# Performance work log

Measured on AMD Instinct MI355X. Metric: run time of the kernel, lower is better.

Reference implementation:

```python
import jax, jax.numpy as jnp
import numpy as np

# Neuron hyperparameters (mid-range of the optuna search space)
THRESHOLD = 1.0
CURRENT_DECAY = 0.3
VOLTAGE_DECAY = 0.8
TAU_GRAD = 0.5
SCALE_GRAD = 1.0

B, N_IN, H, N_OUT, T = 64, 2048, 1024, 2, 128
SPIKE_RATE = 0.1  # input spike density


@jax.custom_vjp
def spike_fn(v):
    # Heaviside spike with SLAYER exponential surrogate gradient
    return (v >= 0.0).astype(v.dtype)

def _spike_fwd(v):
    return spike_fn(v), v

def _spike_bwd(v, g):
    return (g * SCALE_GRAD * jnp.exp(-jnp.abs(v) / TAU_GRAD),)

spike_fn.defvjp(_spike_fwd, _spike_bwd)


def cuba_dense(spike, W):
    """One SLAYER CUBA Dense block: dense synapse + leaky IF neuron over time.
    spike: [B, N_in, T], W: [N_out, N_in] -> [B, N_out, T] output spikes."""
    z = jnp.einsum('oi,bit->tbo', W, spike)  # synaptic current input, [T, B, O]
    O = W.shape[0]
    zeros = jnp.zeros((spike.shape[0], O), spike.dtype)

    def step(carry, z_t):
        cur, vol = carry
        cur = cur * (1.0 - CURRENT_DECAY) + z_t          # current dynamics
        vol = vol * (1.0 - VOLTAGE_DECAY) + cur          # voltage dynamics
        s = spike_fn(vol - THRESHOLD)                    # threshold spike
        vol = vol * (1.0 - s)                            # reset to zero on spike
        return (cur, vol), s

    _, s = jax.lax.scan(step, (zeros, zeros), z)
    return jnp.transpose(s, (1, 2, 0))  # [B, O, T]


def setup_inputs() -> dict:
    key = jax.random.key(0)
    k0, k1, k2, k3 = jax.random.split(key, 4)
    spike = (jax.random.uniform(k0, (B, N_IN, T)) < SPIKE_RATE).astype(jnp.float32)
    W1 = jax.random.normal(k1, (H, N_IN), jnp.float32) / np.sqrt(N_IN).astype(np.float32)
    W2 = jax.random.normal(k2, (H, H), jnp.float32) / np.sqrt(H).astype(np.float32)
    W3 = jax.random.normal(k3, (N_OUT, H), jnp.float32) / np.sqrt(H).astype(np.float32)
    return {"spike": spike, "W1": W1, "W2": W2, "W3": W3}


def reference(spike, W1, W2, W3):
    s = cuba_dense(spike, W1)
    s = cuba_dense(s, W2)
    s = cuba_dense(s, W3)
    return s  # [B, 2, T]
```

## Files before the change

### kernel.cpp

```cpp
#include <hip/hip_runtime.h>


typedef unsigned short ushort_t;
typedef unsigned int uint_t;
typedef __bf16 bf16x8 __attribute__((ext_vector_type(8)));
typedef float f32x4 __attribute__((ext_vector_type(4)));

#define O_TOT 1024

__device__ __forceinline__ void glds16(const ushort_t* g, ushort_t* l) {
  __builtin_amdgcn_global_load_lds(
      (const __attribute__((address_space(1))) uint_t*)g,
      (__attribute__((address_space(3))) uint_t*)l, 16, 0, 0);
}

__device__ __forceinline__ ushort_t f32_to_bf16_rne(float f) {
  uint_t u = __float_as_uint(f);
  u += 0x7FFFu + ((u >> 16) & 1u);
  return (ushort_t)(u >> 16);
}

__global__ __launch_bounds__(256) void prep(const float* __restrict__ W1,
                                            const float* __restrict__ W2,
                                            const float* __restrict__ spike,
                                            ushort_t* __restrict__ h1,
                                            ushort_t* __restrict__ l1,
                                            ushort_t* __restrict__ h2,
                                            ushort_t* __restrict__ l2,
                                            ushort_t* __restrict__ A1) {
  const int tid = threadIdx.x;
  if (blockIdx.x < 12288) {
    const float* W;
    ushort_t *hp, *lp;
    int idx, K;
    if (blockIdx.x < 8192) {
      idx = blockIdx.x * 256 + tid;
      W = W1; hp = h1; lp = l1; K = 2048;
    } else {
      idx = (blockIdx.x - 8192) * 256 + tid;
      W = W2; hp = h2; lp = l2; K = 1024;
    }
    int e = idx & 7, fr = (idx >> 3) & 15, q = (idx >> 7) & 3;
    int kk = (idx >> 9) & 1, j = (idx >> 10) & 1, qn = (idx >> 11) & 1;
    int rest = idx >> 12;
    int kcm = (K == 2048) ? 31 : 15;
    int kcs = (K == 2048) ? 5 : 4;
    int kc = rest & kcm, o_blk = rest >> kcs;
    int o = o_blk * 64 + qn * 32 + j * 16 + fr;
    int k = kc * 64 + kk * 32 + q * 8 + e;
    float w = W[(size_t)o * K + k];
    ushort_t h = f32_to_bf16_rne(w);
    hp[idx] = h;
    lp[idx] = f32_to_bf16_rne(w - __uint_as_float(((uint_t)h) << 16));
    return;
  }
  __shared__ ushort_t lds[128 * 130];
  const int bid = blockIdx.x - 12288;
  const int b = bid >> 4;
  const int i0 = (bid & 15) * 128;
#pragma unroll
  for (int it = 0; it < 16; ++it) {
    int p = it * 256 + tid;
    int i = p >> 5, tg = (p & 31) * 4;
    float4 v = *(const float4*)(spike + ((size_t)b * 2048 + i0 + i) * 128 + tg);
    lds[i * 130 + tg + 0] = (v.x != 0.0f) ? 0x3F80u : 0u;
    lds[i * 130 + tg + 1] = (v.y != 0.0f) ? 0x3F80u : 0u;
    lds[i * 130 + tg + 2] = (v.z != 0.0f) ? 0x3F80u : 0u;
    lds[i * 130 + tg + 3] = (v.w != 0.0f) ? 0x3F80u : 0u;
  }
  __syncthreads();
#pragma unroll
  for (int it = 0; it < 16; ++it) {
    int p = it * 256 + tid;
    int t = p >> 5, j = p & 31;
    uint_t u0 = (uint_t)lds[(4 * j + 0) * 130 + t] | ((uint_t)lds[(4 * j + 1) * 130 + t] << 16);
    uint_t u1 = (uint_t)lds[(4 * j + 2) * 130 + t] | ((uint_t)lds[(4 * j + 3) * 130 + t] << 16);
    uint2* dst = (uint2*)(A1 + (size_t)(b * 128 + t) * 2048 + i0);
    dst[j] = make_uint2(u0, u1);
  }
}

__global__ __launch_bounds__(256, 4)
void gemm_scan(const ushort_t* __restrict__ A, const ushort_t* __restrict__ Bhp,
               const ushort_t* __restrict__ Blp, ushort_t* __restrict__ S,
               int K) {
  __shared__ float smemf[128 * 65];
  ushort_t* As = (ushort_t*)smemf;
  float* Zt = smemf;

  const int tid = threadIdx.x;
  const int wave = tid >> 6, lane = tid & 63;
  const int b = blockIdx.y;
  const int m0 = b * 128;
  const int o0 = blockIdx.x * 64;
  const int qm = wave >> 1, qn = wave & 1;
  const int fr = lane & 15, q = lane >> 4;

  f32x4 acc[4][2];
#pragma unroll
  for (int i = 0; i < 4; ++i)
#pragma unroll
    for (int j = 0; j < 2; ++j) acc[i][j] = (f32x4){0.f, 0.f, 0.f, 0.f};

  size_t gA[4];
  ushort_t* lA[4];
#pragma unroll
  for (int r = 0; r < 4; ++r) {
    int s = wave * 256 + r * 64 + lane;
    int row = s >> 3;
    int u = (s & 7) ^ (row & 7);
    gA[r] = (size_t)(m0 + row) * K + u * 8;
    lA[r] = As + (size_t)(wave * 256 + r * 64) * 8;
  }

  int aoff[4][2];
#pragma unroll
  for (int i = 0; i < 4; ++i)
#pragma unroll
    for (int kk = 0; kk < 2; ++kk) {
      int row = qm * 64 + i * 16 + fr;
      aoff[i][kk] = row * 64 + (((kk * 4 + q) ^ (row & 7))) * 8;
    }

  const size_t pbase = ((size_t)blockIdx.x * (K >> 6)) * 4096 + qn * 2048 + lane * 8;
  const ushort_t* pBh = Bhp + pbase;
  const ushort_t* pBl = Blp + pbase;

  for (int kc = 0; kc < K; kc += 64) {
    bf16x8 bh[2][2], bl[2][2];
    const ushort_t* ph = pBh + (size_t)(kc >> 6) * 4096;
    const ushort_t* pl = pBl + (size_t)(kc >> 6) * 4096;
#pragma unroll
    for (int j = 0; j < 2; ++j)
#pragma unroll
      for (int kk = 0; kk < 2; ++kk) {
        bh[j][kk] = *(const bf16x8*)(ph + j * 1024 + kk * 512);
        bl[j][kk] = *(const bf16x8*)(pl + j * 1024 + kk * 512);
      }
#pragma unroll
    for (int r = 0; r < 4; ++r) glds16(A + gA[r] + kc, lA[r]);
    __syncthreads();

#pragma unroll
    for (int kk = 0; kk < 2; ++kk) {
      bf16x8 af[4];
#pragma unroll
      for (int i = 0; i < 4; ++i) af[i] = *(const bf16x8*)(As + aoff[i][kk]);
#pragma unroll
      for (int i = 0; i < 4; ++i)
#pragma unroll
        for (int j = 0; j < 2; ++j) {
          acc[i][j] = __builtin_amdgcn_mfma_f32_16x16x32_bf16(af[i], bh[j][kk], acc[i][j], 0, 0, 0);
          acc[i][j] = __builtin_amdgcn_mfma_f32_16x16x32_bf16(af[i], bl[j][kk], acc[i][j], 0, 0, 0);
        }
    }
    __syncthreads();
  }

#pragma unroll
  for (int i = 0; i < 4; ++i)
#pragma unroll
    for (int j = 0; j < 2; ++j)
#pragma unroll
      for (int rr = 0; rr < 4; ++rr)
        Zt[(qm * 64 + i * 16 + q * 4 + rr) * 65 + qn * 32 + j * 16 + fr] = acc[i][j][rr];
  __syncthreads();

  if (tid < 64) {
#pragma clang fp contract(off)
    float cur = 0.0f, vol = 0.0f;
    const int o = o0 + tid;
    for (int t = 0; t < 128; ++t) {
      float z = Zt[t * 65 + tid];
      cur = cur * 0.7f;
      cur = cur + z;
      vol = vol * 0.2f;
      vol = vol + cur;
      float v = vol - 1.0f;
      float s = (v >= 0.0f) ? 1.0f : 0.0f;
      vol = vol * (1.0f - s);
      S[(size_t)(m0 + t) * O_TOT + o] = (v >= 0.0f) ? 0x3F80u : 0u;
    }
  }
}

__global__ __launch_bounds__(256) void gemm3_scan(const ushort_t* __restrict__ X,
                                                  const float* __restrict__ W3,
                                                  float* __restrict__ out) {
  __shared__ float w3s[2048];
  __shared__ float z3[256];
  __shared__ float sp[256];
  const int tid = threadIdx.x;
  const int b = blockIdx.x;
  for (int i = tid; i < 2048; i += 256) w3s[i] = W3[i];
  __syncthreads();
  const int wave = tid >> 6, lane = tid & 63;
  for (int tt = 0; tt < 32; ++tt) {
    int t = wave * 32 + tt;
    const uint_t* row = (const uint_t*)(X + (size_t)(b * 128 + t) * 1024) + lane * 8;
    float s0 = 0.0f, s1 = 0.0f;
#pragma unroll
    for (int jw = 0; jw < 8; ++jw) {
      uint_t u = row[jw];
      float x0 = __uint_as_float(u << 16);
      float x1 = __uint_as_float(u & 0xFFFF0000u);
      int i0 = lane * 16 + jw * 2;
      s0 = fmaf(x0, w3s[i0], s0);
      s1 = fmaf(x0, w3s[1024 + i0], s1);
      s0 = fmaf(x1, w3s[i0 + 1], s0);
      s1 = fmaf(x1, w3s[1024 + i0 + 1], s1);
    }
#pragma unroll
    for (int off = 32; off > 0; off >>= 1) {
      s0 += __shfl_down(s0, off);
      s1 += __shfl_down(s1, off);
    }
    if (lane == 0) {
      z3[t * 2] = s0;
      z3[t * 2 + 1] = s1;
    }
  }
  __syncthreads();
  if (tid < 2) {
#pragma clang fp contract(off)
    float cur = 0.0f, vol = 0.0f;
    for (int t = 0; t < 128; ++t) {
      float z = z3[t * 2 + tid];
      cur = cur * 0.7f;
      cur = cur + z;
      vol = vol * 0.2f;
      vol = vol + cur;
      float v = vol - 1.0f;
      float s = (v >= 0.0f) ? 1.0f : 0.0f;
      vol = vol * (1.0f - s);
      sp[tid * 128 + t] = s;
    }
  }
  __syncthreads();
  out[b * 256 + tid] = sp[tid];
}

extern "C" void kernel_launch(void* const* d_in, const int* in_sizes, int n_in,
                              void* d_out, int out_size, void* d_ws, size_t ws_size,
                              hipStream_t stream) {
  const float* spike = (const float*)d_in[0];
  const float* W1 = (const float*)d_in[1];
  const float* W2 = (const float*)d_in[2];
  const float* W3 = (const float*)d_in[3];
  float* out = (float*)d_out;

  char* ws = (char*)d_ws;
  ushort_t* A1 = (ushort_t*)ws;
  ushort_t* S2 = (ushort_t*)(ws + (size_t)32 * 1024 * 1024);
  ushort_t* S3 = (ushort_t*)(ws + (size_t)48 * 1024 * 1024);
  ushort_t* W1hi = (ushort_t*)(ws + (size_t)64 * 1024 * 1024);
  ushort_t* W1lo = (ushort_t*)(ws + (size_t)68 * 1024 * 1024);
  ushort_t* W2hi = (ushort_t*)(ws + (size_t)72 * 1024 * 1024);
  ushort_t* W2lo = (ushort_t*)(ws + (size_t)74 * 1024 * 1024);

  prep<<<13312, 256, 0, stream>>>(W1, W2, spike, W1hi, W1lo, W2hi, W2lo, A1);
  gemm_scan<<<dim3(16, 64), 256, 0, stream>>>(A1, W1hi, W1lo, S2, 2048);
  gemm_scan<<<dim3(16, 64), 256, 0, stream>>>(S2, W2hi, W2lo, S3, 1024);
  gemm3_scan<<<64, 256, 0, stream>>>(S3, W3, out);
}
```

Measured before the change: 251.5 us.

## Switch spike GEMMs to int8 MFMA with three-plane weight decomposition

Binary spike activations are stored as uint8 instead of bf16, and weights are split into three int8 fixed-point planes (scales 2^-8, 2^-15, 2^-22) instead of bf16 hi/lo pairs. The GEMMs use i32 16x16x64 int8 MFMA and recombine the planes in fp32 before the scan. This halves activation bytes and raises MFMA throughput. The trade-offs are three MFMAs per tile instead of two, output tiles shrinking to 32 columns, and exactness that now depends on weight magnitude fitting the int8 range (|w|<0.5) and on quantization residuals small enough not to flip spike thresholds.

New measurement: 236.7 us. -5.9%, faster.

```diff
diff --git a/kernel.cpp b/kernel.cpp
--- a/kernel.cpp
+++ b/kernel.cpp
@@ -3,59 +3,62 @@
 
 typedef unsigned short ushort_t;
 typedef unsigned int uint_t;
-typedef __bf16 bf16x8 __attribute__((ext_vector_type(8)));
-typedef float f32x4 __attribute__((ext_vector_type(4)));
-
-#define O_TOT 1024
-
-__device__ __forceinline__ void glds16(const ushort_t* g, ushort_t* l) {
+typedef unsigned char uchar_t;
+typedef int i32x4 __attribute__((ext_vector_type(4)));
+
+#define S1F 0.00390625f
+#define S2F 3.0517578125e-5f
+#define S3F 2.384185791015625e-7f
+
+__device__ __forceinline__ void glds16(const uchar_t* g, uchar_t* l) {
   __builtin_amdgcn_global_load_lds(
       (const __attribute__((address_space(1))) uint_t*)g,
       (__attribute__((address_space(3))) uint_t*)l, 16, 0, 0);
 }
 
-__device__ __forceinline__ ushort_t f32_to_bf16_rne(float f) {
-  uint_t u = __float_as_uint(f);
-  u += 0x7FFFu + ((u >> 16) & 1u);
-  return (ushort_t)(u >> 16);
-}
-
 __global__ __launch_bounds__(256) void prep(const float* __restrict__ W1,
                                             const float* __restrict__ W2,
                                             const float* __restrict__ spike,
-                                            ushort_t* __restrict__ h1,
-                                            ushort_t* __restrict__ l1,
-                                            ushort_t* __restrict__ h2,
-                                            ushort_t* __restrict__ l2,
-                                            ushort_t* __restrict__ A1) {
+                                            char* __restrict__ w1q1,
+                                            char* __restrict__ w1q2,
+                                            char* __restrict__ w1q3,
+                                            char* __restrict__ w2q1,
+                                            char* __restrict__ w2q2,
+                                            char* __restrict__ w2q3,
+                                            uchar_t* __restrict__ A1) {
   const int tid = threadIdx.x;
-  if (blockIdx.x < 12288) {
+  if (blockIdx.x < 3072) {
     const float* W;
-    ushort_t *hp, *lp;
-    int idx, K;
-    if (blockIdx.x < 8192) {
-      idx = blockIdx.x * 256 + tid;
-      W = W1; hp = h1; lp = l1; K = 2048;
+    char *p1, *p2, *p3;
+    size_t e0;
+    if (blockIdx.x < 2048) {
+      W = W1; p1 = w1q1; p2 = w1q2; p3 = w1q3;
+      e0 = (size_t)blockIdx.x * 1024 + tid * 4;
     } else {
-      idx = (blockIdx.x - 8192) * 256 + tid;
-      W = W2; hp = h2; lp = l2; K = 1024;
-    }
-    int e = idx & 7, fr = (idx >> 3) & 15, q = (idx >> 7) & 3;
-    int kk = (idx >> 9) & 1, j = (idx >> 10) & 1, qn = (idx >> 11) & 1;
-    int rest = idx >> 12;
-    int kcm = (K == 2048) ? 31 : 15;
-    int kcs = (K == 2048) ? 5 : 4;
-    int kc = rest & kcm, o_blk = rest >> kcs;
-    int o = o_blk * 64 + qn * 32 + j * 16 + fr;
-    int k = kc * 64 + kk * 32 + q * 8 + e;
-    float w = W[(size_t)o * K + k];
-    ushort_t h = f32_to_bf16_rne(w);
-    hp[idx] = h;
-    lp[idx] = f32_to_bf16_rne(w - __uint_as_float(((uint_t)h) << 16));
+      W = W2; p1 = w2q1; p2 = w2q2; p3 = w2q3;
+      e0 = (size_t)(blockIdx.x - 2048) * 1024 + tid * 4;
+    }
+    float4 w = *(const float4*)(W + e0);
+    char4 c1, c2, c3;
+    float q, r;
+#define QUANT(comp, f1, f2, f3)                    \
+    q = rintf((comp) * 256.0f);  f1 = (char)(int)q; \
+    r = (comp) - q * S1F;                           \
+    q = rintf(r * 32768.0f);     f2 = (char)(int)q; \
+    r = r - q * S2F;                                \
+    q = rintf(r * 4194304.0f);   f3 = (char)(int)q;
+    QUANT(w.x, c1.x, c2.x, c3.x)
+    QUANT(w.y, c1.y, c2.y, c3.y)
+    QUANT(w.z, c1.z, c2.z, c3.z)
+    QUANT(w.w, c1.w, c2.w, c3.w)
+#undef QUANT
+    *(char4*)(p1 + e0) = c1;
+    *(char4*)(p2 + e0) = c2;
+    *(char4*)(p3 + e0) = c3;
     return;
   }
-  __shared__ ushort_t lds[128 * 130];
-  const int bid = blockIdx.x - 12288;
+  __shared__ uchar_t lds8[128 * 132];
+  const int bid = blockIdx.x - 3072;
   const int b = bid >> 4;
   const int i0 = (bid & 15) * 128;
 #pragma unroll
@@ -63,115 +66,116 @@
     int p = it * 256 + tid;
     int i = p >> 5, tg = (p & 31) * 4;
     float4 v = *(const float4*)(spike + ((size_t)b * 2048 + i0 + i) * 128 + tg);
-    lds[i * 130 + tg + 0] = (v.x != 0.0f) ? 0x3F80u : 0u;
-    lds[i * 130 + tg + 1] = (v.y != 0.0f) ? 0x3F80u : 0u;
-    lds[i * 130 + tg + 2] = (v.z != 0.0f) ? 0x3F80u : 0u;
-    lds[i * 130 + tg + 3] = (v.w != 0.0f) ? 0x3F80u : 0u;
+    uint_t pk = (v.x != 0.0f ? 1u : 0u) | (v.y != 0.0f ? 1u : 0u) << 8 |
+                (v.z != 0.0f ? 1u : 0u) << 16 | (v.w != 0.0f ? 1u : 0u) << 24;
+    *(uint_t*)(lds8 + i * 132 + tg) = pk;
   }
   __syncthreads();
 #pragma unroll
   for (int it = 0; it < 16; ++it) {
     int p = it * 256 + tid;
-    int t = p >> 5, j = p & 31;
-    uint_t u0 = (uint_t)lds[(4 * j + 0) * 130 + t] | ((uint_t)lds[(4 * j + 1) * 130 + t] << 16);
-    uint_t u1 = (uint_t)lds[(4 * j + 2) * 130 + t] | ((uint_t)lds[(4 * j + 3) * 130 + t] << 16);
-    uint2* dst = (uint2*)(A1 + (size_t)(b * 128 + t) * 2048 + i0);
-    dst[j] = make_uint2(u0, u1);
+    int t = p >> 5, jw = p & 31;
+    uint_t u = (uint_t)lds8[(4 * jw + 0) * 132 + t] |
+               ((uint_t)lds8[(4 * jw + 1) * 132 + t] << 8) |
+               ((uint_t)lds8[(4 * jw + 2) * 132 + t] << 16) |
+               ((uint_t)lds8[(4 * jw + 3) * 132 + t] << 24);
+    *(uint_t*)(A1 + (size_t)(b * 128 + t) * 2048 + i0 + jw * 4) = u;
   }
 }
 
 __global__ __launch_bounds__(256, 4)
-void gemm_scan(const ushort_t* __restrict__ A, const ushort_t* __restrict__ Bhp,
-               const ushort_t* __restrict__ Blp, ushort_t* __restrict__ S,
-               int K) {
-  __shared__ float smemf[128 * 65];
-  ushort_t* As = (ushort_t*)smemf;
+void gemm_scan(const uchar_t* __restrict__ A, const char* __restrict__ Q1,
+               const char* __restrict__ Q2, const char* __restrict__ Q3,
+               uchar_t* __restrict__ S, int K) {
+  __shared__ float smemf[128 * 33];
+  uchar_t* sA = (uchar_t*)smemf;
   float* Zt = smemf;
 
   const int tid = threadIdx.x;
   const int wave = tid >> 6, lane = tid & 63;
-  const int b = blockIdx.y;
-  const int m0 = b * 128;
-  const int o0 = blockIdx.x * 64;
+  const int m0 = blockIdx.y * 128;
+  const int o0 = blockIdx.x * 32;
   const int qm = wave >> 1, qn = wave & 1;
   const int fr = lane & 15, q = lane >> 4;
 
-  f32x4 acc[4][2];
+  i32x4 acc[4][3];
 #pragma unroll
   for (int i = 0; i < 4; ++i)
 #pragma unroll
-    for (int j = 0; j < 2; ++j) acc[i][j] = (f32x4){0.f, 0.f, 0.f, 0.f};
-
-  size_t gA[4];
-  ushort_t* lA[4];
-#pragma unroll
-  for (int r = 0; r < 4; ++r) {
-    int s = wave * 256 + r * 64 + lane;
-    int row = s >> 3;
-    int u = (s & 7) ^ (row & 7);
-    gA[r] = (size_t)(m0 + row) * K + u * 8;
-    lA[r] = As + (size_t)(wave * 256 + r * 64) * 8;
-  }
-
-  int aoff[4][2];
+    for (int p = 0; p < 3; ++p) acc[i][p] = (i32x4){0, 0, 0, 0};
+
+  const char* qplanes[3] = {Q1, Q2, Q3};
+  const uchar_t* gsrc[4];
+  uchar_t* ldst[4];
+#pragma unroll
+  for (int it = 0; it < 4; ++it) {
+    int s = it * 256 + tid;
+    gsrc[it] = nullptr;
+    if (s < 896) {
+      ldst[it] = sA + (size_t)(it * 256 + wave * 64) * 16;
+      if (s < 512) {
+        int row = s >> 2, pu = s & 3;
+        int u = pu ^ ((row >> 1) & 3);
+        gsrc[it] = A + (size_t)(m0 + row) * K + u * 16;
+      } else {
+        int t2 = s - 512;
+        int p = t2 >> 7, r = t2 & 127;
+        int row = r >> 2, pu = r & 3;
+        int u = pu ^ ((row >> 1) & 3);
+        gsrc[it] = (const uchar_t*)qplanes[p] + (size_t)(o0 + row) * K + u * 16;
+      }
+    }
+  }
+
+  int aoff[4], boff[3];
+#pragma unroll
+  for (int i = 0; i < 4; ++i) {
+    int row = qm * 64 + i * 16 + fr;
+    aoff[i] = (row * 4 + (q ^ ((row >> 1) & 3))) * 16;
+  }
+  {
+    int row = qn * 16 + fr;
+    int phys = (row * 4 + (q ^ ((row >> 1) & 3))) * 16;
+#pragma unroll
+    for (int p = 0; p < 3; ++p) boff[p] = 8192 + p * 2048 + phys;
+  }
+
+  for (int kc = 0; kc < K; kc += 64) {
+#pragma unroll
+    for (int it = 0; it < 4; ++it)
+      if (gsrc[it]) glds16(gsrc[it] + kc, ldst[it]);
+    __syncthreads();
+
+    i32x4 af[4], bq[3];
+#pragma unroll
+    for (int i = 0; i < 4; ++i) af[i] = *(const i32x4*)(sA + aoff[i]);
+#pragma unroll
+    for (int p = 0; p < 3; ++p) bq[p] = *(const i32x4*)(sA + boff[p]);
+#pragma unroll
+    for (int p = 0; p < 3; ++p)
+#pragma unroll
+      for (int i = 0; i < 4; ++i)
+        acc[i][p] = __builtin_amdgcn_mfma_i32_16x16x64_i8(af[i], bq[p], acc[i][p], 0, 0, 0);
+    __syncthreads();
+  }
+
 #pragma unroll
   for (int i = 0; i < 4; ++i)
 #pragma unroll
-    for (int kk = 0; kk < 2; ++kk) {
-      int row = qm * 64 + i * 16 + fr;
-      aoff[i][kk] = row * 64 + (((kk * 4 + q) ^ (row & 7))) * 8;
-    }
-
-  const size_t pbase = ((size_t)blockIdx.x * (K >> 6)) * 4096 + qn * 2048 + lane * 8;
-  const ushort_t* pBh = Bhp + pbase;
-  const ushort_t* pBl = Blp + pbase;
-
-  for (int kc = 0; kc < K; kc += 64) {
-    bf16x8 bh[2][2], bl[2][2];
-    const ushort_t* ph = pBh + (size_t)(kc >> 6) * 4096;
-    const ushort_t* pl = pBl + (size_t)(kc >> 6) * 4096;
-#pragma unroll
-    for (int j = 0; j < 2; ++j)
-#pragma unroll
-      for (int kk = 0; kk < 2; ++kk) {
-        bh[j][kk] = *(const bf16x8*)(ph + j * 1024 + kk * 512);
-        bl[j][kk] = *(const bf16x8*)(pl + j * 1024 + kk * 512);
-      }
-#pragma unroll
-    for (int r = 0; r < 4; ++r) glds16(A + gA[r] + kc, lA[r]);
-    __syncthreads();
-
-#pragma unroll
-    for (int kk = 0; kk < 2; ++kk) {
-      bf16x8 af[4];
-#pragma unroll
-      for (int i = 0; i < 4; ++i) af[i] = *(const bf16x8*)(As + aoff[i][kk]);
-#pragma unroll
-      for (int i = 0; i < 4; ++i)
-#pragma unroll
-        for (int j = 0; j < 2; ++j) {
-          acc[i][j] = __builtin_amdgcn_mfma_f32_16x16x32_bf16(af[i], bh[j][kk], acc[i][j], 0, 0, 0);
-          acc[i][j] = __builtin_amdgcn_mfma_f32_16x16x32_bf16(af[i], bl[j][kk], acc[i][j], 0, 0, 0);
-        }
-    }
-    __syncthreads();
-  }
-
-#pragma unroll
-  for (int i = 0; i < 4; ++i)
-#pragma unroll
-    for (int j = 0; j < 2; ++j)
-#pragma unroll
-      for (int rr = 0; rr < 4; ++rr)
-        Zt[(qm * 64 + i * 16 + q * 4 + rr) * 65 + qn * 32 + j * 16 + fr] = acc[i][j][rr];
-  __syncthreads();
-
-  if (tid < 64) {
+    for (int rr = 0; rr < 4; ++rr) {
+      int t = qm * 64 + i * 16 + q * 4 + rr;
+      float z = (float)acc[i][0][rr] * S1F + (float)acc[i][1][rr] * S2F +
+                (float)acc[i][2][rr] * S3F;
+      Zt[t * 33 + qn * 16 + fr] = z;
+    }
+  __syncthreads();
+
+  if (tid < 32) {
 #pragma clang fp contract(off)
     float cur = 0.0f, vol = 0.0f;
     const int o = o0 + tid;
     for (int t = 0; t < 128; ++t) {
-      float z = Zt[t * 65 + tid];
+      float z = Zt[t * 33 + tid];
       cur = cur * 0.7f;
       cur = cur + z;
       vol = vol * 0.2f;
@@ -179,12 +183,12 @@
       float v = vol - 1.0f;
       float s = (v >= 0.0f) ? 1.0f : 0.0f;
       vol = vol * (1.0f - s);
-      S[(size_t)(m0 + t) * O_TOT + o] = (v >= 0.0f) ? 0x3F80u : 0u;
-    }
-  }
-}
-
-__global__ __launch_bounds__(256) void gemm3_scan(const ushort_t* __restrict__ X,
+      S[(size_t)(m0 + t) * 1024 + o] = (v >= 0.0f) ? 1u : 0u;
+    }
+  }
+}
+
+__global__ __launch_bounds__(256) void gemm3_scan(const uchar_t* __restrict__ X,
                                                   const float* __restrict__ W3,
                                                   float* __restrict__ out) {
   __shared__ float w3s[2048];
@@ -197,19 +201,19 @@
   const int wave = tid >> 6, lane = tid & 63;
   for (int tt = 0; tt < 32; ++tt) {
     int t = wave * 32 + tt;
-    const uint_t* row = (const uint_t*)(X + (size_t)(b * 128 + t) * 1024) + lane * 8;
+    const uint4* rp = (const uint4*)(X + (size_t)(b * 128 + t) * 1024);
+    uint4 v = rp[lane];
     float s0 = 0.0f, s1 = 0.0f;
-#pragma unroll
-    for (int jw = 0; jw < 8; ++jw) {
-      uint_t u = row[jw];
-      float x0 = __uint_as_float(u << 16);
-      float x1 = __uint_as_float(u & 0xFFFF0000u);
-      int i0 = lane * 16 + jw * 2;
-      s0 = fmaf(x0, w3s[i0], s0);
-      s1 = fmaf(x0, w3s[1024 + i0], s1);
-      s0 = fmaf(x1, w3s[i0 + 1], s0);
-      s1 = fmaf(x1, w3s[1024 + i0 + 1], s1);
-    }
+    const uint_t uw[4] = {v.x, v.y, v.z, v.w};
+#pragma unroll
+    for (int wq = 0; wq < 4; ++wq)
+#pragma unroll
+      for (int c = 0; c < 4; ++c) {
+        float x = (float)((uw[wq] >> (8 * c)) & 1u);
+        int i0 = lane * 16 + wq * 4 + c;
+        s0 = fmaf(x, w3s[i0], s0);
+        s1 = fmaf(x, w3s[1024 + i0], s1);
+      }
 #pragma unroll
     for (int off = 32; off > 0; off >>= 1) {
       s0 += __shfl_down(s0, off);
@@ -250,16 +254,20 @@
   float* out = (float*)d_out;
 
   char* ws = (char*)d_ws;
-  ushort_t* A1 = (ushort_t*)ws;
-  ushort_t* S2 = (ushort_t*)(ws + (size_t)32 * 1024 * 1024);
-  ushort_t* S3 = (ushort_t*)(ws + (size_t)48 * 1024 * 1024);
-  ushort_t* W1hi = (ushort_t*)(ws + (size_t)64 * 1024 * 1024);
-  ushort_t* W1lo = (ushort_t*)(ws + (size_t)68 * 1024 * 1024);
-  ushort_t* W2hi = (ushort_t*)(ws + (size_t)72 * 1024 * 1024);
-  ushort_t* W2lo = (ushort_t*)(ws + (size_t)74 * 1024 * 1024);
-
-  prep<<<13312, 256, 0, stream>>>(W1, W2, spike, W1hi, W1lo, W2hi, W2lo, A1);
-  gemm_scan<<<dim3(16, 64), 256, 0, stream>>>(A1, W1hi, W1lo, S2, 2048);
-  gemm_scan<<<dim3(16, 64), 256, 0, stream>>>(S2, W2hi, W2lo, S3, 1024);
+  const size_t MB = 1024 * 1024;
+  uchar_t* A1 = (uchar_t*)ws;
+  uchar_t* S2 = (uchar_t*)(ws + 16 * MB);
+  uchar_t* S3 = (uchar_t*)(ws + 24 * MB);
+  char* w1q1 = ws + 32 * MB;
+  char* w1q2 = ws + 34 * MB;
+  char* w1q3 = ws + 36 * MB;
+  char* w2q1 = ws + 38 * MB;
+  char* w2q2 = ws + 39 * MB;
+  char* w2q3 = ws + 40 * MB;
+
+  prep<<<4096, 256, 0, stream>>>(W1, W2, spike, w1q1, w1q2, w1q3, w2q1, w2q2,
+                                 w2q3, A1);
+  gemm_scan<<<dim3(32, 64), 256, 0, stream>>>(A1, w1q1, w1q2, w1q3, S2, 2048);
+  gemm_scan<<<dim3(32, 64), 256, 0, stream>>>(S2, w2q1, w2q2, w2q3, S3, 1024);
   gemm3_scan<<<64, 256, 0, stream>>>(S3, W3, out);
 }
```
